# Performance work log

Hardware: AMD Instinct MI355X
Metric: run time of the kernel (lower is better)

## Reference

```python
import jax, jax.numpy as jnp
import numpy as np

B, S, L, F = 32, 48, 64, 256


def setup_inputs() -> dict:
    key = jax.random.key(0)
    ks = jax.random.split(key, 7)
    return {
        "features": jax.random.normal(ks[0], (B, S, L, F), dtype=jnp.float32),
        "src_locs": jax.random.normal(ks[1], (B, L, 2), dtype=jnp.float32),
        "tar_locs": jax.random.normal(ks[2], (B, 2), dtype=jnp.float32),
        "W1": jax.random.normal(ks[3], (F, F), dtype=jnp.float32) * (1.0 / np.sqrt(F)),
        "b1": jax.random.normal(ks[4], (F,), dtype=jnp.float32) * 0.02,
        "W2": jax.random.normal(ks[5], (F, 1), dtype=jnp.float32) * (1.0 / np.sqrt(F)),
        "b2": jax.random.normal(ks[6], (1,), dtype=jnp.float32) * 0.02,
    }


def reference(features, src_locs, tar_locs, W1, b1, W2, b2):
    # features: (B, S, L, F); src_locs: (B, L, 2); tar_locs: (B, 2)
    # MLP score: Linear(F,F) + ReLU + Linear(F,1) + ReLU -> (B, S, L, 1)
    attn = jax.nn.relu(jnp.einsum('bslf,fg->bslg', features, W1) + b1)
    attn = jax.nn.relu(jnp.einsum('bslf,fo->bslo', attn, W2) + b2)  # (B,S,L,1)
    # inverse-distance weights over stations: (B, L)
    dists = jnp.sqrt(jnp.sum((src_locs - tar_locs[:, None, :]) ** 2, axis=-1))
    inv_dists = 1.0 / dists  # (B, L)
    # broadcast to (B, 1, L, 1), softmax over src_length axis (axis=2)
    attn_scores = jax.nn.softmax(attn * inv_dists[:, None, :, None], axis=2)
    # weighted sum over stations -> (B, S, F)
    return jnp.sum(features * attn_scores, axis=2)
```

## Files before the change

### kernel.cpp

```cpp
#include <hip/hip_runtime.h>
#include <hip/hip_fp16.h>
#include <math.h>

typedef _Float16 half8 __attribute__((ext_vector_type(8)));
typedef float floatx4 __attribute__((ext_vector_type(4)));

#define BB 32
#define SS 48
#define LL 64
#define FF 256
#define NSLICE 2
#define NBLK ((BB * SS) / NSLICE)

#define WAVE_BARRIER() do {                                          \
    asm volatile("s_waitcnt lgkmcnt(0)" ::: "memory");               \
    __builtin_amdgcn_s_barrier();                                    \
    asm volatile("" ::: "memory");                                   \
} while (0)

#define ISSUE_FENCE() asm volatile("" ::: "memory")

template <int CTRL>
__device__ __forceinline__ float dpp_add(float x) {
    int y = __builtin_amdgcn_update_dpp(0, __float_as_int(x), CTRL, 0xF, 0xF, true);
    return x + __int_as_float(y);
}
template <int CTRL>
__device__ __forceinline__ float dpp_max(float x) {
    int y = __builtin_amdgcn_update_dpp(0, __float_as_int(x), CTRL, 0xF, 0xF, true);
    return fmaxf(x, __int_as_float(y));
}
__device__ __forceinline__ float row16_sum(float x) {
    x = dpp_add<0xB1>(x);
    x = dpp_add<0x4E>(x);
    x = dpp_add<0x124>(x);
    x = dpp_add<0x128>(x);
    return x;
}
__device__ __forceinline__ float row16_max(float x) {
    x = dpp_max<0xB1>(x);
    x = dpp_max<0x4E>(x);
    x = dpp_max<0x124>(x);
    x = dpp_max<0x128>(x);
    return x;
}

__global__ __launch_bounds__(256) void prep_w(const float* __restrict__ W1,
                                              _Float16* __restrict__ whi) {
    int idx = blockIdx.x * 256 + threadIdx.x;
    int j    = idx & 7;
    int lane = (idx >> 3) & 63;
    int nt   = (idx >> 9) & 15;
    int kt   = idx >> 13;
    int k = kt * 32 + ((lane >> 4) & 3) * 8 + j;
    int n = nt * 16 + (lane & 15);
    whi[idx] = (_Float16)W1[k * FF + n];
}

__global__ __launch_bounds__(512, 6) void ida_mfma(
    const float* __restrict__ features,
    const float* __restrict__ src_locs,
    const float* __restrict__ tar_locs,
    const _Float16* __restrict__ whi,
    const float* __restrict__ b1,
    const float* __restrict__ W2,
    const float* __restrict__ b2,
    float* __restrict__ out)
{
    __shared__ _Float16 Ahi[16384];
    __shared__ float SP[8 * LL];

    const int t    = threadIdx.x;
    const int w    = t >> 6;
    const int lane = t & 63;
    const int quad = lane >> 4;
    const int l16  = lane & 15;
    const int g    = blockIdx.x;
    const int b    = (g * NSLICE) / SS;

    float sx = src_locs[(b * LL + lane) * 2 + 0];
    float sy = src_locs[(b * LL + lane) * 2 + 1];
    float tx = tar_locs[b * 2 + 0];
    float ty = tar_locs[b * 2 + 1];
    float b2v = b2[0];
    float b1v[2], w2v[2];
    #pragma unroll
    for (int ntl = 0; ntl < 2; ++ntl) {
        int n = (w * 2 + ntl) * 16 + l16;
        b1v[ntl] = b1[n];
        w2v[ntl] = W2[n];
    }
    ISSUE_FENCE();

    float4 araw[8];
    {
        const float* Xg0 = features + (size_t)(g * NSLICE) * (LL * FF);
        #pragma unroll
        for (int it = 0; it < 4; ++it) {
            const float4* p = (const float4*)(Xg0 + (it * 16 + l16) * FF + w * 32 + quad * 8);
            araw[2 * it + 0] = p[0];
            araw[2 * it + 1] = p[1];
        }
    }
    ISSUE_FENCE();

    #pragma unroll
    for (int i = 0; i < NSLICE; ++i) {
        const int bs = g * NSLICE + i;

        #pragma unroll
        for (int it = 0; it < 4; ++it) {
            int G = it * 8 + w;
            float4 x0 = araw[2 * it + 0], x1 = araw[2 * it + 1];
            float xs[8] = {x0.x, x0.y, x0.z, x0.w, x1.x, x1.y, x1.z, x1.w};
            half8 hi;
            #pragma unroll
            for (int j = 0; j < 8; ++j) hi[j] = (_Float16)xs[j];
            *((half8*)&Ahi[(G * 64 + lane) * 8]) = hi;
        }

        half8 bq[3][2];
        #pragma unroll
        for (int c = 0; c < 2; ++c)
            #pragma unroll
            for (int ntl = 0; ntl < 2; ++ntl)
                bq[c][ntl] = *((const half8*)(whi + ((size_t)(c * 16 + (w * 2 + ntl)) * 64 + lane) * 8));
        ISSUE_FENCE();

        WAVE_BARRIER();

        floatx4 acc[4][2] = {};

        #pragma unroll
        for (int kt = 0; kt < 8; ++kt) {
            if (kt < 6) {
                #pragma unroll
                for (int ntl = 0; ntl < 2; ++ntl)
                    bq[(kt + 2) % 3][ntl] = *((const half8*)(whi + ((size_t)((kt + 2) * 16 + (w * 2 + ntl)) * 64 + lane) * 8));
            }
            #pragma unroll
            for (int mt = 0; mt < 4; ++mt) {
                half8 ahi = *((half8*)&Ahi[((mt * 8 + kt) * 64 + lane) * 8]);
                #pragma unroll
                for (int ntl = 0; ntl < 2; ++ntl)
                    acc[mt][ntl] = __builtin_amdgcn_mfma_f32_16x16x32_f16(ahi, bq[kt % 3][ntl], acc[mt][ntl], 0, 0, 0);
            }
        }

        if (i + 1 < NSLICE) {
            const float* Xgn = features + (size_t)(bs + 1) * (LL * FF);
            #pragma unroll
            for (int it = 0; it < 4; ++it) {
                const float4* p = (const float4*)(Xgn + (it * 16 + l16) * FF + w * 32 + quad * 8);
                araw[2 * it + 0] = p[0];
                araw[2 * it + 1] = p[1];
            }
            ISSUE_FENCE();
        }

        #pragma unroll
        for (int mt = 0; mt < 4; ++mt) {
            #pragma unroll
            for (int r = 0; r < 4; ++r) {
                float p = 0.f;
                #pragma unroll
                for (int ntl = 0; ntl < 2; ++ntl) {
                    float h = fmaxf(acc[mt][ntl][r] + b1v[ntl], 0.f);
                    p = fmaf(h, w2v[ntl], p);
                }
                p = row16_sum(p);
                if (l16 == 0) SP[w * LL + mt * 16 + quad * 4 + r] = p;
            }
        }

        WAVE_BARRIER();

        float s = SP[0 * LL + lane] + SP[1 * LL + lane] + SP[2 * LL + lane] + SP[3 * LL + lane]
                + SP[4 * LL + lane] + SP[5 * LL + lane] + SP[6 * LL + lane] + SP[7 * LL + lane] + b2v;
        float score = fmaxf(s, 0.f);
        float dxv = sx - tx, dyv = sy - ty;
        float inv_d = 1.0f / sqrtf(dxv * dxv + dyv * dyv);
        float logit = score * inv_d;
        float m = row16_max(logit);
        m = fmaxf(m, __shfl_xor(m, 16));
        m = fmaxf(m, __shfl_xor(m, 32));
        float e = __expf(logit - m);
        float se = row16_sum(e);
        se += __shfl_xor(se, 16);
        se += __shfl_xor(se, 32);
        float wgt = e / se;

        float o8[8] = {0.f, 0.f, 0.f, 0.f, 0.f, 0.f, 0.f, 0.f};
        #pragma unroll
        for (int it = 0; it < 4; ++it) {
            float wr = __shfl(wgt, it * 16 + l16);
            half8 hv = *((half8*)&Ahi[((it * 8 + w) * 64 + lane) * 8]);
            #pragma unroll
            for (int j = 0; j < 8; ++j)
                o8[j] = fmaf((float)hv[j], wr, o8[j]);
        }
        #pragma unroll
        for (int j = 0; j < 8; ++j)
            o8[j] = row16_sum(o8[j]);
        if (l16 == 0) {
            float* op = out + (size_t)bs * FF + w * 32 + quad * 8;
            float4 s0 = {o8[0], o8[1], o8[2], o8[3]};
            float4 s1 = {o8[4], o8[5], o8[6], o8[7]};
            *((float4*)op) = s0;
            *((float4*)(op + 4)) = s1;
        }

        if (i + 1 < NSLICE)
            WAVE_BARRIER();
    }
}

extern "C" void kernel_launch(void* const* d_in, const int* in_sizes, int n_in,
                              void* d_out, int out_size, void* d_ws, size_t ws_size,
                              hipStream_t stream) {
    const float* features = (const float*)d_in[0];
    const float* src_locs = (const float*)d_in[1];
    const float* tar_locs = (const float*)d_in[2];
    const float* W1       = (const float*)d_in[3];
    const float* b1       = (const float*)d_in[4];
    const float* W2       = (const float*)d_in[5];
    const float* b2       = (const float*)d_in[6];
    float* out = (float*)d_out;

    _Float16* whi = (_Float16*)d_ws;

    prep_w<<<dim3(FF * FF / 256), dim3(256), 0, stream>>>(W1, whi);
    ida_mfma<<<dim3(NBLK), dim3(512), 0, stream>>>(
        features, src_locs, tar_locs, whi, b1, W2, b2, out);
}
```

Before: 188.7 us.

## Double-buffer feature registers, weight sum from fp32 regs, three slices per block

The kernel keeps two register buffers of raw fp32 features so the weighted-sum stage reads the current slice's fp32 values instead of re-reading fp16 data from shared memory. This also makes the final output accumulate in full precision. The trailing barrier between slices is dropped, slices per block go from 2 to 3, and launch bounds move from 6 to 4 waves-per-EU occupancy to make room for the extra registers. The goal is fewer LDS reads and barriers and more prefetch overlap. The cost is higher register pressure and fewer resident blocks. Dropping the barrier may also let the next slice's LDS writes overwrite Ahi while other waves are still in the previous slice's MFMA loop, although the SP sync probably orders this.

```diff
diff --git a/kernel.cpp b/kernel.cpp
--- a/kernel.cpp
+++ b/kernel.cpp
@@ -9,7 +9,7 @@
 #define SS 48
 #define LL 64
 #define FF 256
-#define NSLICE 2
+#define NSLICE 3
 #define NBLK ((BB * SS) / NSLICE)
 
 #define WAVE_BARRIER() do {                                          \
@@ -57,7 +57,7 @@
     whi[idx] = (_Float16)W1[k * FF + n];
 }
 
-__global__ __launch_bounds__(512, 6) void ida_mfma(
+__global__ __launch_bounds__(512, 4) void ida_mfma(
     const float* __restrict__ features,
     const float* __restrict__ src_locs,
     const float* __restrict__ tar_locs,
@@ -92,127 +92,136 @@
     }
     ISSUE_FENCE();
 
-    float4 araw[8];
+    float4 arA[8], arB[8];
+
     {
         const float* Xg0 = features + (size_t)(g * NSLICE) * (LL * FF);
         #pragma unroll
         for (int it = 0; it < 4; ++it) {
             const float4* p = (const float4*)(Xg0 + (it * 16 + l16) * FF + w * 32 + quad * 8);
-            araw[2 * it + 0] = p[0];
-            araw[2 * it + 1] = p[1];
+            arA[2 * it + 0] = p[0];
+            arA[2 * it + 1] = p[1];
         }
     }
     ISSUE_FENCE();
 
-    #pragma unroll
-    for (int i = 0; i < NSLICE; ++i) {
-        const int bs = g * NSLICE + i;
-
-        #pragma unroll
-        for (int it = 0; it < 4; ++it) {
-            int G = it * 8 + w;
-            float4 x0 = araw[2 * it + 0], x1 = araw[2 * it + 1];
-            float xs[8] = {x0.x, x0.y, x0.z, x0.w, x1.x, x1.y, x1.z, x1.w};
-            half8 hi;
-            #pragma unroll
-            for (int j = 0; j < 8; ++j) hi[j] = (_Float16)xs[j];
-            *((half8*)&Ahi[(G * 64 + lane) * 8]) = hi;
-        }
-
-        half8 bq[3][2];
-        #pragma unroll
-        for (int c = 0; c < 2; ++c)
-            #pragma unroll
-            for (int ntl = 0; ntl < 2; ++ntl)
-                bq[c][ntl] = *((const half8*)(whi + ((size_t)(c * 16 + (w * 2 + ntl)) * 64 + lane) * 8));
-        ISSUE_FENCE();
-
-        WAVE_BARRIER();
-
-        floatx4 acc[4][2] = {};
-
-        #pragma unroll
-        for (int kt = 0; kt < 8; ++kt) {
-            if (kt < 6) {
-                #pragma unroll
-                for (int ntl = 0; ntl < 2; ++ntl)
-                    bq[(kt + 2) % 3][ntl] = *((const half8*)(whi + ((size_t)((kt + 2) * 16 + (w * 2 + ntl)) * 64 + lane) * 8));
-            }
-            #pragma unroll
-            for (int mt = 0; mt < 4; ++mt) {
-                half8 ahi = *((half8*)&Ahi[((mt * 8 + kt) * 64 + lane) * 8]);
-                #pragma unroll
-                for (int ntl = 0; ntl < 2; ++ntl)
-                    acc[mt][ntl] = __builtin_amdgcn_mfma_f32_16x16x32_f16(ahi, bq[kt % 3][ntl], acc[mt][ntl], 0, 0, 0);
-            }
-        }
-
-        if (i + 1 < NSLICE) {
-            const float* Xgn = features + (size_t)(bs + 1) * (LL * FF);
-            #pragma unroll
-            for (int it = 0; it < 4; ++it) {
-                const float4* p = (const float4*)(Xgn + (it * 16 + l16) * FF + w * 32 + quad * 8);
-                araw[2 * it + 0] = p[0];
-                araw[2 * it + 1] = p[1];
-            }
-            ISSUE_FENCE();
-        }
-
-        #pragma unroll
-        for (int mt = 0; mt < 4; ++mt) {
-            #pragma unroll
-            for (int r = 0; r < 4; ++r) {
-                float p = 0.f;
-                #pragma unroll
-                for (int ntl = 0; ntl < 2; ++ntl) {
-                    float h = fmaxf(acc[mt][ntl][r] + b1v[ntl], 0.f);
-                    p = fmaf(h, w2v[ntl], p);
-                }
-                p = row16_sum(p);
-                if (l16 == 0) SP[w * LL + mt * 16 + quad * 4 + r] = p;
-            }
-        }
-
-        WAVE_BARRIER();
-
-        float s = SP[0 * LL + lane] + SP[1 * LL + lane] + SP[2 * LL + lane] + SP[3 * LL + lane]
-                + SP[4 * LL + lane] + SP[5 * LL + lane] + SP[6 * LL + lane] + SP[7 * LL + lane] + b2v;
-        float score = fmaxf(s, 0.f);
-        float dxv = sx - tx, dyv = sy - ty;
-        float inv_d = 1.0f / sqrtf(dxv * dxv + dyv * dyv);
-        float logit = score * inv_d;
-        float m = row16_max(logit);
-        m = fmaxf(m, __shfl_xor(m, 16));
-        m = fmaxf(m, __shfl_xor(m, 32));
-        float e = __expf(logit - m);
-        float se = row16_sum(e);
-        se += __shfl_xor(se, 16);
-        se += __shfl_xor(se, 32);
-        float wgt = e / se;
-
-        float o8[8] = {0.f, 0.f, 0.f, 0.f, 0.f, 0.f, 0.f, 0.f};
-        #pragma unroll
-        for (int it = 0; it < 4; ++it) {
-            float wr = __shfl(wgt, it * 16 + l16);
-            half8 hv = *((half8*)&Ahi[((it * 8 + w) * 64 + lane) * 8]);
-            #pragma unroll
-            for (int j = 0; j < 8; ++j)
-                o8[j] = fmaf((float)hv[j], wr, o8[j]);
-        }
-        #pragma unroll
-        for (int j = 0; j < 8; ++j)
-            o8[j] = row16_sum(o8[j]);
-        if (l16 == 0) {
-            float* op = out + (size_t)bs * FF + w * 32 + quad * 8;
-            float4 s0 = {o8[0], o8[1], o8[2], o8[3]};
-            float4 s1 = {o8[4], o8[5], o8[6], o8[7]};
-            *((float4*)op) = s0;
-            *((float4*)(op + 4)) = s1;
-        }
-
-        if (i + 1 < NSLICE)
-            WAVE_BARRIER();
+#define SLICE_BODY(i, CUR, NXT)                                                   \
+    {                                                                             \
+        const int bs = g * NSLICE + (i);                                          \
+         \
+        _Pragma("unroll")                                                         \
+        for (int it = 0; it < 4; ++it) {                                          \
+            int G = it * 8 + w;                                                   \
+            float4 x0 = CUR[2 * it + 0], x1 = CUR[2 * it + 1];                    \
+            float xs[8] = {x0.x, x0.y, x0.z, x0.w, x1.x, x1.y, x1.z, x1.w};       \
+            half8 hi;                                                             \
+            _Pragma("unroll")                                                     \
+            for (int j = 0; j < 8; ++j) hi[j] = (_Float16)xs[j];                  \
+            *((half8*)&Ahi[(G * 64 + lane) * 8]) = hi;                            \
+        }                                                                         \
+                    \
+        half8 bq[3][2];                                                           \
+        _Pragma("unroll")                                                         \
+        for (int c = 0; c < 2; ++c)                                               \
+            _Pragma("unroll")                                                     \
+            for (int ntl = 0; ntl < 2; ++ntl)                                     \
+                bq[c][ntl] = *((const half8*)(whi +                               \
+                    ((size_t)(c * 16 + (w * 2 + ntl)) * 64 + lane) * 8));         \
+        ISSUE_FENCE();                                                            \
+        WAVE_BARRIER();               \
+        floatx4 acc[4][2] = {};                                                   \
+        _Pragma("unroll")                                                         \
+        for (int kt = 0; kt < 8; ++kt) {                                          \
+            if (kt < 6) {                                                         \
+                _Pragma("unroll")                                                 \
+                for (int ntl = 0; ntl < 2; ++ntl)                                 \
+                    bq[(kt + 2) % 3][ntl] = *((const half8*)(whi +                \
+                        ((size_t)((kt + 2) * 16 + (w * 2 + ntl)) * 64 + lane) * 8)); \
+            }                                                                     \
+            _Pragma("unroll")                                                     \
+            for (int mt = 0; mt < 4; ++mt) {                                      \
+                half8 ahi = *((half8*)&Ahi[((mt * 8 + kt) * 64 + lane) * 8]);     \
+                _Pragma("unroll")                                                 \
+                for (int ntl = 0; ntl < 2; ++ntl)                                 \
+                    acc[mt][ntl] = __builtin_amdgcn_mfma_f32_16x16x32_f16(        \
+                        ahi, bq[kt % 3][ntl], acc[mt][ntl], 0, 0, 0);             \
+            }                                                                     \
+        }                                                                         \
+                   \
+        if ((i) + 1 < NSLICE) {                                                   \
+            const float* Xgn = features + (size_t)(bs + 1) * (LL * FF);           \
+            _Pragma("unroll")                                                     \
+            for (int it = 0; it < 4; ++it) {                                      \
+                const float4* p = (const float4*)(Xgn + (it * 16 + l16) * FF      \
+                                                  + w * 32 + quad * 8);           \
+                NXT[2 * it + 0] = p[0];                                           \
+                NXT[2 * it + 1] = p[1];                                           \
+            }                                                                     \
+            ISSUE_FENCE();                                                        \
+        }                                                                         \
+                                         \
+        _Pragma("unroll")                                                         \
+        for (int mt = 0; mt < 4; ++mt) {                                          \
+            _Pragma("unroll")                                                     \
+            for (int r = 0; r < 4; ++r) {                                         \
+                float p = 0.f;                                                    \
+                _Pragma("unroll")                                                 \
+                for (int ntl = 0; ntl < 2; ++ntl) {                               \
+                    float h = fmaxf(acc[mt][ntl][r] + b1v[ntl], 0.f);             \
+                    p = fmaf(h, w2v[ntl], p);                                     \
+                }                                                                 \
+                p = row16_sum(p);                                                 \
+                if (l16 == 0) SP[w * LL + mt * 16 + quad * 4 + r] = p;            \
+            }                                                                     \
+        }                                                                         \
+        WAVE_BARRIER();        \
+                                 \
+        float s = SP[0 * LL + lane] + SP[1 * LL + lane] + SP[2 * LL + lane]       \
+                + SP[3 * LL + lane] + SP[4 * LL + lane] + SP[5 * LL + lane]       \
+                + SP[6 * LL + lane] + SP[7 * LL + lane] + b2v;                    \
+        float score = fmaxf(s, 0.f);                                              \
+        float dxv = sx - tx, dyv = sy - ty;                                       \
+        float inv_d = 1.0f / sqrtf(dxv * dxv + dyv * dyv);                        \
+        float logit = score * inv_d;                                              \
+        float m = row16_max(logit);                                               \
+        m = fmaxf(m, __shfl_xor(m, 16));                                          \
+        m = fmaxf(m, __shfl_xor(m, 32));                                          \
+        float e = __expf(logit - m);                                              \
+        float se = row16_sum(e);                                                  \
+        se += __shfl_xor(se, 16);                                                 \
+        se += __shfl_xor(se, 32);                                                 \
+        float wgt = e / se;                                                       \
+            \
+        float o8[8] = {0.f, 0.f, 0.f, 0.f, 0.f, 0.f, 0.f, 0.f};                   \
+        _Pragma("unroll")                                                         \
+        for (int it = 0; it < 4; ++it) {                                          \
+            float wr = __shfl(wgt, it * 16 + l16);                                \
+            float4 x0 = CUR[2 * it + 0], x1 = CUR[2 * it + 1];                    \
+            o8[0] = fmaf(x0.x, wr, o8[0]);                                        \
+            o8[1] = fmaf(x0.y, wr, o8[1]);                                        \
+            o8[2] = fmaf(x0.z, wr, o8[2]);                                        \
+            o8[3] = fmaf(x0.w, wr, o8[3]);                                        \
+            o8[4] = fmaf(x1.x, wr, o8[4]);                                        \
+            o8[5] = fmaf(x1.y, wr, o8[5]);                                        \
+            o8[6] = fmaf(x1.z, wr, o8[6]);                                        \
+            o8[7] = fmaf(x1.w, wr, o8[7]);                                        \
+        }                                                                         \
+        _Pragma("unroll")                                                         \
+        for (int j = 0; j < 8; ++j)                                               \
+            o8[j] = row16_sum(o8[j]);                                             \
+        if (l16 == 0) {                                                           \
+            float* op = out + (size_t)bs * FF + w * 32 + quad * 8;                \
+            float4 s0 = {o8[0], o8[1], o8[2], o8[3]};                             \
+            float4 s1 = {o8[4], o8[5], o8[6], o8[7]};                             \
+            *((float4*)op) = s0;                                                  \
+            *((float4*)(op + 4)) = s1;                                            \
+        }                                                                         \
     }
+
+    SLICE_BODY(0, arA, arB)
+    SLICE_BODY(1, arB, arA)
+    SLICE_BODY(2, arA, arB)
+#undef SLICE_BODY
 }
 
 extern "C" void kernel_launch(void* const* d_in, const int* in_sizes, int n_in,
```

Measured after the change: 183.6 us. 1.03x faster.
